# Kernel tuning notes

Measured on AMD Instinct MI355X. Metric: run time of the kernel, lower is better.

The kernel has to match this reference:

```python
import jax, jax.numpy as jnp
import numpy as np

B = 512    # batch of signals
N = 1024   # time samples per signal
M = 16384  # frequency grid points (super-resolved)


def setup_inputs() -> dict:
    key = jax.random.key(0)
    x = jax.random.normal(key, (B, 2, N), dtype=jnp.float32)  # [B, 2(re/im), N]
    xgrid = jnp.linspace(-0.5, 0.5, M, dtype=jnp.float32)      # normalized freqs
    return {"x": x, "xgrid": xgrid}


def reference(x, xgrid):
    # x: [B, 2, N] -> complex signal a + i*b
    # Periodogram at arbitrary freqs f: P(f) = |sum_n x_n * exp(-2j*pi*f*n)|^2 / N
    a = x[:, 0]  # real part [B, N]
    b = x[:, 1]  # imag part [B, N]
    Nn = x.shape[-1]
    n = jnp.arange(Nn, dtype=x.dtype)
    phase = (2.0 * jnp.pi) * xgrid[:, None] * n[None, :]  # [M, N]
    C = jnp.cos(phase)  # [M, N]
    S = jnp.sin(phase)  # [M, N]
    # x_n * (cos - i sin) = (a c + b s) + i (b c - a s)
    re = jnp.einsum('bn,mn->bm', a, C) + jnp.einsum('bn,mn->bm', b, S)
    im = jnp.einsum('bn,mn->bm', b, C) - jnp.einsum('bn,mn->bm', a, S)
    return (re * re + im * im) / Nn  # [B, M]
```

## Files before the change

kernel.cpp:

```cpp
#include <hip/hip_runtime.h>


typedef __fp16 half8 __attribute__((ext_vector_type(8)));
typedef __fp16 half2v __attribute__((ext_vector_type(2)));
typedef float f32x4 __attribute__((ext_vector_type(4)));

#define B_SZ 512
#define N_SZ 1024
#define M_SZ 16384
#define BT 128
#define MT 128
#define KT 32

union U2  { half2v h2[2]; uint2 u; };
union H8U { half8 v; uint4 u; };

__global__ __launch_bounds__(256, 2)
void periodogram_kernel(const float* __restrict__ x, const float* __restrict__ xgrid,
                        float* __restrict__ out) {
    __shared__ __align__(16) unsigned char smem[4 * 8192];
    const int tid  = (int)threadIdx.x;
    const int lane = tid & 63;
    const int w    = tid >> 6;
    const int bid  = (int)blockIdx.x;
    const int b0 = (bid & 3) * BT;
    const int m0 = (bid >> 2) * MT;

    if (((bid ^ (bid >> 8)) & 1) != 0) __builtin_amdgcn_s_sleep(22);

    const int row8 = tid >> 3;
    const int kk   = (tid & 7) * 4;
    const int g    = kk >> 3;
    const int kkh  = (kk >> 2) & 1;

    unsigned woff[4];
    const float* srcA[4];
    float C1[4], S1[4], C32[4], S32[4], c0v[4], s0v[4];
#pragma unroll
    for (int rep = 0; rep < 4; ++rep) {
        const int row = row8 + rep * 32;
        const int rb = row >> 4, r16 = row & 15;
        woff[rep] = (unsigned)(rb * 1024 + ((g * 16 + (r16 ^ (g << 1))) << 4) + kkh * 8);
        srcA[rep] = x + (size_t)(b0 + row) * 2048 + kk;
        const float xg = xgrid[m0 + row];
        const float f1 = xg - floorf(xg);
        C1[rep] = __builtin_amdgcn_cosf(f1);
        S1[rep] = __builtin_amdgcn_sinf(f1);
        float p32 = xg * 32.0f; p32 -= floorf(p32);
        C32[rep] = __builtin_amdgcn_cosf(p32);
        S32[rep] = __builtin_amdgcn_sinf(p32);
        const float kf = (float)kk;
        const float pk = xg * kf;
        const float e  = __builtin_fmaf(xg, kf, -pk);
        const float f  = (pk - floorf(pk)) + e;
        c0v[rep] = __builtin_amdgcn_cosf(f);
        s0v[rep] = __builtin_amdgcn_sinf(f);
    }

    f32x4 accRe[4][4], accIm[4][4];
#pragma unroll
    for (int i = 0; i < 4; ++i)
#pragma unroll
        for (int j = 0; j < 4; ++j) { accRe[i][j] = (f32x4)0.0f; accIm[i][j] = (f32x4)0.0f; }

    const int wr = (w >> 1) * 64;
    const int wc = (w & 1) * 64;
    const unsigned roff  = (unsigned)((lane ^ ((lane >> 4) << 1)) << 4);
    const unsigned aBase = 0u     + ((unsigned)(wr >> 4) << 10) + roff;
    const unsigned bBase = 8192u  + ((unsigned)(wr >> 4) << 10) + roff;
    const unsigned cBase = 16384u + ((unsigned)(wc >> 4) << 10) + roff;
    const unsigned sBase = 24576u + ((unsigned)(wc >> 4) << 10) + roff;

    for (int t = 0; t < N_SZ / KT; ++t) {
        const int k0 = t * KT;
        float4 va[4], vb[4];
#pragma unroll
        for (int rep = 0; rep < 4; ++rep) {
            va[rep] = *(const float4*)(srcA[rep] + k0);
            vb[rep] = *(const float4*)(srcA[rep] + k0 + 1024);
        }
        uint2 cw[4], sw[4];
#pragma unroll
        for (int rep = 0; rep < 4; ++rep) {
            const float c0 = c0v[rep], s0 = s0v[rep];
            const float c1 = __builtin_fmaf(c0, C1[rep], -(s0 * S1[rep]));
            const float s1 = __builtin_fmaf(s0, C1[rep],  (c0 * S1[rep]));
            const float c2 = __builtin_fmaf(c1, C1[rep], -(s1 * S1[rep]));
            const float s2 = __builtin_fmaf(s1, C1[rep],  (c1 * S1[rep]));
            const float c3 = __builtin_fmaf(c2, C1[rep], -(s2 * S1[rep]));
            const float s3 = __builtin_fmaf(s2, C1[rep],  (c2 * S1[rep]));
            U2 pc, ps;
            pc.h2[0] = __builtin_amdgcn_cvt_pkrtz(c0, c1);
            pc.h2[1] = __builtin_amdgcn_cvt_pkrtz(c2, c3);
            ps.h2[0] = __builtin_amdgcn_cvt_pkrtz(s0, s1);
            ps.h2[1] = __builtin_amdgcn_cvt_pkrtz(s2, s3);
            cw[rep] = pc.u; sw[rep] = ps.u;
            c0v[rep] = __builtin_fmaf(c0, C32[rep], -(s0 * S32[rep]));
            s0v[rep] = __builtin_fmaf(s0, C32[rep],  (c0 * S32[rep]));
        }
        __syncthreads();
#pragma unroll
        for (int rep = 0; rep < 4; ++rep) {
            U2 pa, pb;
            pa.h2[0] = __builtin_amdgcn_cvt_pkrtz(va[rep].x, va[rep].y);
            pa.h2[1] = __builtin_amdgcn_cvt_pkrtz(va[rep].z, va[rep].w);
            pb.h2[0] = __builtin_amdgcn_cvt_pkrtz(vb[rep].x, vb[rep].y);
            pb.h2[1] = __builtin_amdgcn_cvt_pkrtz(vb[rep].z, vb[rep].w);
            *(uint2*)(smem + 0     + woff[rep]) = pa.u;
            *(uint2*)(smem + 8192  + woff[rep]) = pb.u;
            *(uint2*)(smem + 16384 + woff[rep]) = cw[rep];
            *(uint2*)(smem + 24576 + woff[rep]) = sw[rep];
        }
        __syncthreads();
        half8 fa[4], fb[4];
#pragma unroll
        for (int fm = 0; fm < 4; ++fm) {
            fa[fm] = *(const half8*)(smem + aBase + fm * 1024);
            fb[fm] = *(const half8*)(smem + bBase + fm * 1024);
        }
#pragma unroll
        for (int fn = 0; fn < 4; ++fn) {
            const half8 fc = *(const half8*)(smem + cBase + fn * 1024);
            H8U fsU;  fsU.v = *(const half8*)(smem + sBase + fn * 1024);
            H8U fnsU;
            fnsU.u.x = fsU.u.x ^ 0x80008000u;
            fnsU.u.y = fsU.u.y ^ 0x80008000u;
            fnsU.u.z = fsU.u.z ^ 0x80008000u;
            fnsU.u.w = fsU.u.w ^ 0x80008000u;
#pragma unroll
            for (int fm = 0; fm < 4; ++fm) {
                accRe[fm][fn] = __builtin_amdgcn_mfma_f32_16x16x32_f16(fa[fm], fc,     accRe[fm][fn], 0, 0, 0);
                accRe[fm][fn] = __builtin_amdgcn_mfma_f32_16x16x32_f16(fb[fm], fsU.v,  accRe[fm][fn], 0, 0, 0);
                accIm[fm][fn] = __builtin_amdgcn_mfma_f32_16x16x32_f16(fb[fm], fc,     accIm[fm][fn], 0, 0, 0);
                accIm[fm][fn] = __builtin_amdgcn_mfma_f32_16x16x32_f16(fa[fm], fnsU.v, accIm[fm][fn], 0, 0, 0);
            }
        }
    }

    const float inv = 1.0f / (float)N_SZ;
    const int orow0 = b0 + wr + ((lane >> 4) << 2);
    const int ocol0 = m0 + wc + (lane & 15);
#pragma unroll
    for (int fm = 0; fm < 4; ++fm)
#pragma unroll
        for (int fn = 0; fn < 4; ++fn) {
            const f32x4 r = accRe[fm][fn];
            const f32x4 im = accIm[fm][fn];
            const int col = ocol0 + fn * 16;
#pragma unroll
            for (int j = 0; j < 4; ++j) {
                const int row = orow0 + fm * 16 + j;
                out[(size_t)row * M_SZ + col] = (r[j] * r[j] + im[j] * im[j]) * inv;
            }
        }
}

extern "C" void kernel_launch(void* const* d_in, const int* in_sizes, int n_in,
                              void* d_out, int out_size, void* d_ws, size_t ws_size,
                              hipStream_t stream) {
    const float* x     = (const float*)d_in[0];
    const float* xgrid = (const float*)d_in[1];
    float* out = (float*)d_out;
    dim3 grid(B_SZ / BT * (M_SZ / MT));
    dim3 block(256);
    periodogram_kernel<<<grid, block, 0, stream>>>(x, xgrid, out);
}
```

Measured before the change: 67.96 us.

## Double-buffer LDS tiles to overlap next-tile loads and twiddle generation with MFMA

```diff
diff --git a/kernel.cpp b/kernel.cpp
--- a/kernel.cpp
+++ b/kernel.cpp
@@ -11,6 +11,7 @@
 #define BT 128
 #define MT 128
 #define KT 32
+#define BUF 32768u
 
 union U2  { half2v h2[2]; uint2 u; };
 union H8U { half8 v; uint4 u; };
@@ -18,15 +19,13 @@
 __global__ __launch_bounds__(256, 2)
 void periodogram_kernel(const float* __restrict__ x, const float* __restrict__ xgrid,
                         float* __restrict__ out) {
-    __shared__ __align__(16) unsigned char smem[4 * 8192];
+    __shared__ __align__(16) unsigned char smem[2 * BUF];
     const int tid  = (int)threadIdx.x;
     const int lane = tid & 63;
     const int w    = tid >> 6;
     const int bid  = (int)blockIdx.x;
     const int b0 = (bid & 3) * BT;
     const int m0 = (bid >> 2) * MT;
-
-    if (((bid ^ (bid >> 8)) & 1) != 0) __builtin_amdgcn_s_sleep(22);
 
     const int row8 = tid >> 3;
     const int kk   = (tid & 7) * 4;
@@ -71,17 +70,11 @@
     const unsigned cBase = 16384u + ((unsigned)(wc >> 4) << 10) + roff;
     const unsigned sBase = 24576u + ((unsigned)(wc >> 4) << 10) + roff;
 
-    for (int t = 0; t < N_SZ / KT; ++t) {
-        const int k0 = t * KT;
-        float4 va[4], vb[4];
+    {
 #pragma unroll
         for (int rep = 0; rep < 4; ++rep) {
-            va[rep] = *(const float4*)(srcA[rep] + k0);
-            vb[rep] = *(const float4*)(srcA[rep] + k0 + 1024);
-        }
-        uint2 cw[4], sw[4];
-#pragma unroll
-        for (int rep = 0; rep < 4; ++rep) {
+            const float4 va = *(const float4*)(srcA[rep]);
+            const float4 vb = *(const float4*)(srcA[rep] + 1024);
             const float c0 = c0v[rep], s0 = s0v[rep];
             const float c1 = __builtin_fmaf(c0, C1[rep], -(s0 * S1[rep]));
             const float s1 = __builtin_fmaf(s0, C1[rep],  (c0 * S1[rep]));
@@ -89,39 +82,67 @@
             const float s2 = __builtin_fmaf(s1, C1[rep],  (c1 * S1[rep]));
             const float c3 = __builtin_fmaf(c2, C1[rep], -(s2 * S1[rep]));
             const float s3 = __builtin_fmaf(s2, C1[rep],  (c2 * S1[rep]));
-            U2 pc, ps;
+            U2 pa, pb, pc, ps;
+            pa.h2[0] = __builtin_amdgcn_cvt_pkrtz(va.x, va.y);
+            pa.h2[1] = __builtin_amdgcn_cvt_pkrtz(va.z, va.w);
+            pb.h2[0] = __builtin_amdgcn_cvt_pkrtz(vb.x, vb.y);
+            pb.h2[1] = __builtin_amdgcn_cvt_pkrtz(vb.z, vb.w);
             pc.h2[0] = __builtin_amdgcn_cvt_pkrtz(c0, c1);
             pc.h2[1] = __builtin_amdgcn_cvt_pkrtz(c2, c3);
             ps.h2[0] = __builtin_amdgcn_cvt_pkrtz(s0, s1);
             ps.h2[1] = __builtin_amdgcn_cvt_pkrtz(s2, s3);
-            cw[rep] = pc.u; sw[rep] = ps.u;
+            *(uint2*)(smem + 0     + woff[rep]) = pa.u;
+            *(uint2*)(smem + 8192  + woff[rep]) = pb.u;
+            *(uint2*)(smem + 16384 + woff[rep]) = pc.u;
+            *(uint2*)(smem + 24576 + woff[rep]) = ps.u;
             c0v[rep] = __builtin_fmaf(c0, C32[rep], -(s0 * S32[rep]));
             s0v[rep] = __builtin_fmaf(s0, C32[rep],  (c0 * S32[rep]));
         }
-        __syncthreads();
-#pragma unroll
-        for (int rep = 0; rep < 4; ++rep) {
-            U2 pa, pb;
-            pa.h2[0] = __builtin_amdgcn_cvt_pkrtz(va[rep].x, va[rep].y);
-            pa.h2[1] = __builtin_amdgcn_cvt_pkrtz(va[rep].z, va[rep].w);
-            pb.h2[0] = __builtin_amdgcn_cvt_pkrtz(vb[rep].x, vb[rep].y);
-            pb.h2[1] = __builtin_amdgcn_cvt_pkrtz(vb[rep].z, vb[rep].w);
-            *(uint2*)(smem + 0     + woff[rep]) = pa.u;
-            *(uint2*)(smem + 8192  + woff[rep]) = pb.u;
-            *(uint2*)(smem + 16384 + woff[rep]) = cw[rep];
-            *(uint2*)(smem + 24576 + woff[rep]) = sw[rep];
-        }
-        __syncthreads();
+    }
+    __syncthreads();
+
+    for (int t = 0; t < N_SZ / KT; ++t) {
+        const unsigned cur = (unsigned)(t & 1) * BUF;
+        const unsigned nxt = cur ^ BUF;
+        const bool haveNext = (t < N_SZ / KT - 1);
+        float4 va[4], vb[4];
+        if (haveNext) {
+            const int k0 = (t + 1) * KT;
+#pragma unroll
+            for (int rep = 0; rep < 4; ++rep) {
+                va[rep] = *(const float4*)(srcA[rep] + k0);
+                vb[rep] = *(const float4*)(srcA[rep] + k0 + 1024);
+            }
+#pragma unroll
+            for (int rep = 0; rep < 4; ++rep) {
+                const float c0 = c0v[rep], s0 = s0v[rep];
+                const float c1 = __builtin_fmaf(c0, C1[rep], -(s0 * S1[rep]));
+                const float s1 = __builtin_fmaf(s0, C1[rep],  (c0 * S1[rep]));
+                const float c2 = __builtin_fmaf(c1, C1[rep], -(s1 * S1[rep]));
+                const float s2 = __builtin_fmaf(s1, C1[rep],  (c1 * S1[rep]));
+                const float c3 = __builtin_fmaf(c2, C1[rep], -(s2 * S1[rep]));
+                const float s3 = __builtin_fmaf(s2, C1[rep],  (c2 * S1[rep]));
+                U2 pc, ps;
+                pc.h2[0] = __builtin_amdgcn_cvt_pkrtz(c0, c1);
+                pc.h2[1] = __builtin_amdgcn_cvt_pkrtz(c2, c3);
+                ps.h2[0] = __builtin_amdgcn_cvt_pkrtz(s0, s1);
+                ps.h2[1] = __builtin_amdgcn_cvt_pkrtz(s2, s3);
+                *(uint2*)(smem + nxt + 16384 + woff[rep]) = pc.u;
+                *(uint2*)(smem + nxt + 24576 + woff[rep]) = ps.u;
+                c0v[rep] = __builtin_fmaf(c0, C32[rep], -(s0 * S32[rep]));
+                s0v[rep] = __builtin_fmaf(s0, C32[rep],  (c0 * S32[rep]));
+            }
+        }
         half8 fa[4], fb[4];
 #pragma unroll
         for (int fm = 0; fm < 4; ++fm) {
-            fa[fm] = *(const half8*)(smem + aBase + fm * 1024);
-            fb[fm] = *(const half8*)(smem + bBase + fm * 1024);
+            fa[fm] = *(const half8*)(smem + cur + aBase + fm * 1024);
+            fb[fm] = *(const half8*)(smem + cur + bBase + fm * 1024);
         }
 #pragma unroll
         for (int fn = 0; fn < 4; ++fn) {
-            const half8 fc = *(const half8*)(smem + cBase + fn * 1024);
-            H8U fsU;  fsU.v = *(const half8*)(smem + sBase + fn * 1024);
+            const half8 fc = *(const half8*)(smem + cur + cBase + fn * 1024);
+            H8U fsU;  fsU.v = *(const half8*)(smem + cur + sBase + fn * 1024);
             H8U fnsU;
             fnsU.u.x = fsU.u.x ^ 0x80008000u;
             fnsU.u.y = fsU.u.y ^ 0x80008000u;
@@ -134,6 +155,19 @@
                 accIm[fm][fn] = __builtin_amdgcn_mfma_f32_16x16x32_f16(fb[fm], fc,     accIm[fm][fn], 0, 0, 0);
                 accIm[fm][fn] = __builtin_amdgcn_mfma_f32_16x16x32_f16(fa[fm], fnsU.v, accIm[fm][fn], 0, 0, 0);
             }
+        }
+        if (haveNext) {
+#pragma unroll
+            for (int rep = 0; rep < 4; ++rep) {
+                U2 pa, pb;
+                pa.h2[0] = __builtin_amdgcn_cvt_pkrtz(va[rep].x, va[rep].y);
+                pa.h2[1] = __builtin_amdgcn_cvt_pkrtz(va[rep].z, va[rep].w);
+                pb.h2[0] = __builtin_amdgcn_cvt_pkrtz(vb[rep].x, vb[rep].y);
+                pb.h2[1] = __builtin_amdgcn_cvt_pkrtz(vb[rep].z, vb[rep].w);
+                *(uint2*)(smem + nxt + 0    + woff[rep]) = pa.u;
+                *(uint2*)(smem + nxt + 8192 + woff[rep]) = pb.u;
+            }
+            __syncthreads();
         }
     }
 
```

Measured after the change: 67.59 us. Within noise of the previous version (-0.5%).

## Generate twiddle MFMA fragments in registers instead of staging through LDS

Applied to the files above, without the earlier changes.

```diff
diff --git a/kernel.cpp b/kernel.cpp
--- a/kernel.cpp
+++ b/kernel.cpp
@@ -1,9 +1,9 @@
 #include <hip/hip_runtime.h>
 
 
-typedef __fp16 half8 __attribute__((ext_vector_type(8)));
+typedef __fp16 half8  __attribute__((ext_vector_type(8)));
 typedef __fp16 half2v __attribute__((ext_vector_type(2)));
-typedef float f32x4 __attribute__((ext_vector_type(4)));
+typedef float  f32x4  __attribute__((ext_vector_type(4)));
 
 #define B_SZ 512
 #define N_SZ 1024
@@ -12,13 +12,13 @@
 #define MT 128
 #define KT 32
 
-union U2  { half2v h2[2]; uint2 u; };
-union H8U { half8 v; uint4 u; };
+union U2 { half2v h2[2]; uint2 u; };
+union BF { half2v h2[4]; half8 v; uint4 u; };
 
 __global__ __launch_bounds__(256, 2)
 void periodogram_kernel(const float* __restrict__ x, const float* __restrict__ xgrid,
                         float* __restrict__ out) {
-    __shared__ __align__(16) unsigned char smem[4 * 8192];
+    __shared__ __align__(16) unsigned char smem[2 * 8192];
     const int tid  = (int)threadIdx.x;
     const int lane = tid & 63;
     const int w    = tid >> 6;
@@ -26,7 +26,8 @@
     const int b0 = (bid & 3) * BT;
     const int m0 = (bid >> 2) * MT;
 
-    if (((bid ^ (bid >> 8)) & 1) != 0) __builtin_amdgcn_s_sleep(22);
+    const int wr = (w >> 1) * 64;
+    const int wc = (w & 1) * 64;
 
     const int row8 = tid >> 3;
     const int kk   = (tid & 7) * 4;
@@ -35,26 +36,39 @@
 
     unsigned woff[4];
     const float* srcA[4];
-    float C1[4], S1[4], C32[4], S32[4], c0v[4], s0v[4];
 #pragma unroll
     for (int rep = 0; rep < 4; ++rep) {
         const int row = row8 + rep * 32;
         const int rb = row >> 4, r16 = row & 15;
         woff[rep] = (unsigned)(rb * 1024 + ((g * 16 + (r16 ^ (g << 1))) << 4) + kkh * 8);
         srcA[rep] = x + (size_t)(b0 + row) * 2048 + kk;
-        const float xg = xgrid[m0 + row];
-        const float f1 = xg - floorf(xg);
-        C1[rep] = __builtin_amdgcn_cosf(f1);
-        S1[rep] = __builtin_amdgcn_sinf(f1);
+    }
+
+    half2v PC[4][4], PS[4][4];
+    float c0v[4], s0v[4], C32[4], S32[4];
+    const float g8f = (float)((lane >> 4) << 3);
+#pragma unroll
+    for (int fn = 0; fn < 4; ++fn) {
+        const float xg = xgrid[m0 + wc + fn * 16 + (lane & 15)];
+        float Cj[8], Sj[8];
+        Cj[0] = 1.0f; Sj[0] = 0.0f;
+#pragma unroll
+        for (int j = 1; j < 8; ++j) {
+            float p = xg * (float)j; p -= floorf(p);
+            Cj[j] = __builtin_amdgcn_cosf(p);
+            Sj[j] = __builtin_amdgcn_sinf(p);
+        }
+#pragma unroll
+        for (int i = 0; i < 4; ++i) {
+            PC[fn][i] = __builtin_amdgcn_cvt_pkrtz(Cj[2 * i], Cj[2 * i + 1]);
+            PS[fn][i] = __builtin_amdgcn_cvt_pkrtz(Sj[2 * i], Sj[2 * i + 1]);
+        }
         float p32 = xg * 32.0f; p32 -= floorf(p32);
-        C32[rep] = __builtin_amdgcn_cosf(p32);
-        S32[rep] = __builtin_amdgcn_sinf(p32);
-        const float kf = (float)kk;
-        const float pk = xg * kf;
-        const float e  = __builtin_fmaf(xg, kf, -pk);
-        const float f  = (pk - floorf(pk)) + e;
-        c0v[rep] = __builtin_amdgcn_cosf(f);
-        s0v[rep] = __builtin_amdgcn_sinf(f);
+        C32[fn] = __builtin_amdgcn_cosf(p32);
+        S32[fn] = __builtin_amdgcn_sinf(p32);
+        float pb = xg * g8f; pb -= floorf(pb);
+        c0v[fn] = __builtin_amdgcn_cosf(pb);
+        s0v[fn] = __builtin_amdgcn_sinf(pb);
     }
 
     f32x4 accRe[4][4], accIm[4][4];
@@ -63,13 +77,9 @@
 #pragma unroll
         for (int j = 0; j < 4; ++j) { accRe[i][j] = (f32x4)0.0f; accIm[i][j] = (f32x4)0.0f; }
 
-    const int wr = (w >> 1) * 64;
-    const int wc = (w & 1) * 64;
     const unsigned roff  = (unsigned)((lane ^ ((lane >> 4) << 1)) << 4);
-    const unsigned aBase = 0u     + ((unsigned)(wr >> 4) << 10) + roff;
-    const unsigned bBase = 8192u  + ((unsigned)(wr >> 4) << 10) + roff;
-    const unsigned cBase = 16384u + ((unsigned)(wc >> 4) << 10) + roff;
-    const unsigned sBase = 24576u + ((unsigned)(wc >> 4) << 10) + roff;
+    const unsigned aBase = 0u    + ((unsigned)(wr >> 4) << 10) + roff;
+    const unsigned bBase = 8192u + ((unsigned)(wr >> 4) << 10) + roff;
 
     for (int t = 0; t < N_SZ / KT; ++t) {
         const int k0 = t * KT;
@@ -79,25 +89,6 @@
             va[rep] = *(const float4*)(srcA[rep] + k0);
             vb[rep] = *(const float4*)(srcA[rep] + k0 + 1024);
         }
-        uint2 cw[4], sw[4];
-#pragma unroll
-        for (int rep = 0; rep < 4; ++rep) {
-            const float c0 = c0v[rep], s0 = s0v[rep];
-            const float c1 = __builtin_fmaf(c0, C1[rep], -(s0 * S1[rep]));
-            const float s1 = __builtin_fmaf(s0, C1[rep],  (c0 * S1[rep]));
-            const float c2 = __builtin_fmaf(c1, C1[rep], -(s1 * S1[rep]));
-            const float s2 = __builtin_fmaf(s1, C1[rep],  (c1 * S1[rep]));
-            const float c3 = __builtin_fmaf(c2, C1[rep], -(s2 * S1[rep]));
-            const float s3 = __builtin_fmaf(s2, C1[rep],  (c2 * S1[rep]));
-            U2 pc, ps;
-            pc.h2[0] = __builtin_amdgcn_cvt_pkrtz(c0, c1);
-            pc.h2[1] = __builtin_amdgcn_cvt_pkrtz(c2, c3);
-            ps.h2[0] = __builtin_amdgcn_cvt_pkrtz(s0, s1);
-            ps.h2[1] = __builtin_amdgcn_cvt_pkrtz(s2, s3);
-            cw[rep] = pc.u; sw[rep] = ps.u;
-            c0v[rep] = __builtin_fmaf(c0, C32[rep], -(s0 * S32[rep]));
-            s0v[rep] = __builtin_fmaf(s0, C32[rep],  (c0 * S32[rep]));
-        }
         __syncthreads();
 #pragma unroll
         for (int rep = 0; rep < 4; ++rep) {
@@ -106,10 +97,8 @@
             pa.h2[1] = __builtin_amdgcn_cvt_pkrtz(va[rep].z, va[rep].w);
             pb.h2[0] = __builtin_amdgcn_cvt_pkrtz(vb[rep].x, vb[rep].y);
             pb.h2[1] = __builtin_amdgcn_cvt_pkrtz(vb[rep].z, vb[rep].w);
-            *(uint2*)(smem + 0     + woff[rep]) = pa.u;
-            *(uint2*)(smem + 8192  + woff[rep]) = pb.u;
-            *(uint2*)(smem + 16384 + woff[rep]) = cw[rep];
-            *(uint2*)(smem + 24576 + woff[rep]) = sw[rep];
+            *(uint2*)(smem + 0    + woff[rep]) = pa.u;
+            *(uint2*)(smem + 8192 + woff[rep]) = pb.u;
         }
         __syncthreads();
         half8 fa[4], fb[4];
@@ -120,20 +109,28 @@
         }
 #pragma unroll
         for (int fn = 0; fn < 4; ++fn) {
-            const half8 fc = *(const half8*)(smem + cBase + fn * 1024);
-            H8U fsU;  fsU.v = *(const half8*)(smem + sBase + fn * 1024);
-            H8U fnsU;
-            fnsU.u.x = fsU.u.x ^ 0x80008000u;
-            fnsU.u.y = fsU.u.y ^ 0x80008000u;
-            fnsU.u.z = fsU.u.z ^ 0x80008000u;
-            fnsU.u.w = fsU.u.w ^ 0x80008000u;
+            const float c0 = c0v[fn], s0 = s0v[fn];
+            const half2v c0b = __builtin_amdgcn_cvt_pkrtz(c0, c0);
+            const half2v s0b = __builtin_amdgcn_cvt_pkrtz(s0, s0);
+            BF fc, fs, fns;
+#pragma unroll
+            for (int i = 0; i < 4; ++i) {
+                fc.h2[i] = c0b * PC[fn][i] - s0b * PS[fn][i];
+                fs.h2[i] = s0b * PC[fn][i] + c0b * PS[fn][i];
+            }
+            fns.u.x = fs.u.x ^ 0x80008000u;
+            fns.u.y = fs.u.y ^ 0x80008000u;
+            fns.u.z = fs.u.z ^ 0x80008000u;
+            fns.u.w = fs.u.w ^ 0x80008000u;
 #pragma unroll
             for (int fm = 0; fm < 4; ++fm) {
-                accRe[fm][fn] = __builtin_amdgcn_mfma_f32_16x16x32_f16(fa[fm], fc,     accRe[fm][fn], 0, 0, 0);
-                accRe[fm][fn] = __builtin_amdgcn_mfma_f32_16x16x32_f16(fb[fm], fsU.v,  accRe[fm][fn], 0, 0, 0);
-                accIm[fm][fn] = __builtin_amdgcn_mfma_f32_16x16x32_f16(fb[fm], fc,     accIm[fm][fn], 0, 0, 0);
-                accIm[fm][fn] = __builtin_amdgcn_mfma_f32_16x16x32_f16(fa[fm], fnsU.v, accIm[fm][fn], 0, 0, 0);
+                accRe[fm][fn] = __builtin_amdgcn_mfma_f32_16x16x32_f16(fa[fm], fc.v,  accRe[fm][fn], 0, 0, 0);
+                accRe[fm][fn] = __builtin_amdgcn_mfma_f32_16x16x32_f16(fb[fm], fs.v,  accRe[fm][fn], 0, 0, 0);
+                accIm[fm][fn] = __builtin_amdgcn_mfma_f32_16x16x32_f16(fb[fm], fc.v,  accIm[fm][fn], 0, 0, 0);
+                accIm[fm][fn] = __builtin_amdgcn_mfma_f32_16x16x32_f16(fa[fm], fns.v, accIm[fm][fn], 0, 0, 0);
             }
+            c0v[fn] = __builtin_fmaf(c0, C32[fn], -(s0 * S32[fn]));
+            s0v[fn] = __builtin_fmaf(s0, C32[fn],  (c0 * S32[fn]));
         }
     }
 
```

New measurement: 68.93 us. About the same (+1.4%).
